# Kernel optimization log

Measured on AMD Instinct MI355X. Metric: run time of the kernel, lower is better.

## Reference

```python
import jax, jax.numpy as jnp
import numpy as np

DIM = 256
KEY_DIM = 16
NUM_HEADS = 8
ATTN_RATIO = 4
RES = (32, 32)
N = RES[0] * RES[1]            # 1024 tokens
D = ATTN_RATIO * KEY_DIM       # 64 per-head value dim
DH = D * NUM_HEADS             # 512
H_QKV = DH + 2 * KEY_DIM * NUM_HEADS  # 768
BATCH = 32
EPS = 1e-5


def _bias_idxs():
    # relative-position offset index table: idx[i,j] = |dr|*W + |dc| (bijective
    # over the res0*res1 unique abs-offset pairs, matching the gather structure)
    r = np.arange(RES[0])
    c = np.arange(RES[1])
    rr, cc = np.meshgrid(r, c, indexing='ij')
    pr = rr.reshape(-1)  # [N]
    pc = cc.reshape(-1)
    dr = np.abs(pr[:, None] - pr[None, :])
    dc = np.abs(pc[:, None] - pc[None, :])
    return jnp.asarray(dr * RES[1] + dc, dtype=jnp.int32)  # [N, N]


def setup_inputs() -> dict:
    key = jax.random.key(0)
    ks = jax.random.split(key, 8)
    s_in = 1.0 / np.sqrt(DIM)
    s_dh = 1.0 / np.sqrt(DH)
    return {
        'x': jax.random.normal(ks[0], (BATCH, N, DIM), jnp.float32),
        'norm_w': jnp.ones((DIM,), jnp.float32),
        'norm_b': jnp.zeros((DIM,), jnp.float32),
        'qkv_w': jax.random.normal(ks[1], (H_QKV, DIM), jnp.float32) * s_in,
        'qkv_b': jnp.zeros((H_QKV,), jnp.float32),
        'proj_w': jax.random.normal(ks[2], (DIM, DH), jnp.float32) * s_dh,
        'proj_b': jnp.zeros((DIM,), jnp.float32),
        'attn_biases': jax.random.normal(ks[3], (NUM_HEADS, RES[0] * RES[1]), jnp.float32) * 0.02,
        'bias_idxs': _bias_idxs(),
    }


def reference(x, norm_w, norm_b, qkv_w, qkv_b, proj_w, proj_b, attn_biases, bias_idxs):
    b, n, _ = x.shape
    scale = KEY_DIM ** -0.5
    # LayerNorm
    mu = jnp.mean(x, axis=-1, keepdims=True)
    var = jnp.mean(jnp.square(x - mu), axis=-1, keepdims=True)
    xn = (x - mu) * jax.lax.rsqrt(var + EPS) * norm_w + norm_b
    # fused qkv projection
    qkv = xn @ qkv_w.T + qkv_b                       # [b, n, H_QKV]
    qkv = qkv.reshape(b, n, NUM_HEADS, 2 * KEY_DIM + D)
    q = qkv[..., :KEY_DIM]                           # [b, n, h, k]
    k = qkv[..., KEY_DIM:2 * KEY_DIM]
    v = qkv[..., 2 * KEY_DIM:]                       # [b, n, h, d]
    # scores + gathered relative-position bias
    bias = attn_biases[:, bias_idxs]                 # [h, n, n]
    attn = jnp.einsum('bnhk,bmhk->bhnm', q, k) * scale + bias
    attn = jax.nn.softmax(attn, axis=-1)
    out = jnp.einsum('bhnm,bmhd->bnhd', attn, v).reshape(b, n, DH)
    return out @ proj_w.T + proj_b                   # [b, n, DIM]
```

## Files before the change

### kernel.cpp

```cpp
#include <hip/hip_runtime.h>
#include <hip/hip_bf16.h>

typedef __bf16 bf16x8 __attribute__((ext_vector_type(8)));
typedef float f32x16 __attribute__((ext_vector_type(16)));
typedef float f32x8 __attribute__((ext_vector_type(8)));
typedef float f32x2 __attribute__((ext_vector_type(2)));
typedef unsigned int u32;

#define MFMA32(a, b, c) __builtin_amdgcn_mfma_f32_32x32x16_bf16((a), (b), (c), 0, 0, 0)

__device__ __forceinline__ f32x16 zero16() {
  f32x16 z;
#pragma unroll
  for (int i = 0; i < 16; ++i) z[i] = 0.f;
  return z;
}

__device__ __forceinline__ unsigned short bfb(float f) {
  __hip_bfloat16 h = __float2bfloat16(f);
  return __builtin_bit_cast(unsigned short, h);
}
__device__ __forceinline__ u32 pk2(float lo, float hi) {
  return (u32)bfb(lo) | ((u32)bfb(hi) << 16);
}
__device__ __forceinline__ u32 pk2h(float lo, float hi) {
  _Float16 a = (_Float16)lo, b = (_Float16)hi;
  return (u32)__builtin_bit_cast(unsigned short, a) |
         ((u32)__builtin_bit_cast(unsigned short, b) << 16);
}
__device__ __forceinline__ bf16x8 ld8(const unsigned short* p) {
  return *reinterpret_cast<const bf16x8*>(p);
}
__device__ __forceinline__ void gld_lds16(const void* g, void* l) {
  __builtin_amdgcn_global_load_lds((const __attribute__((address_space(1))) void*)g,
                                   (__attribute__((address_space(3))) void*)l, 16, 0, 0);
}

__global__ __launch_bounds__(256, 4) void ln_kernel(const float* __restrict__ x,
                                                    const float* __restrict__ nw,
                                                    const float* __restrict__ nb,
                                                    unsigned short* __restrict__ xn) {
  int w = threadIdx.x >> 6, lane = threadIdx.x & 63;
  size_t row = (size_t)blockIdx.x * 4 + w;
  float4 v = reinterpret_cast<const float4*>(x + row * 256)[lane];
  float s = (v.x + v.y) + (v.z + v.w);
  float q = (v.x * v.x + v.y * v.y) + (v.z * v.z + v.w * v.w);
#pragma unroll
  for (int m = 1; m < 64; m <<= 1) {
    s += __shfl_xor(s, m, 64);
    q += __shfl_xor(q, m, 64);
  }
  float mu = s * (1.f / 256.f);
  float var = fmaxf(q * (1.f / 256.f) - mu * mu, 0.f);
  float rs = rsqrtf(var + 1e-5f);
  float4 wv = reinterpret_cast<const float4*>(nw)[lane];
  float4 bv = reinterpret_cast<const float4*>(nb)[lane];
  float o0 = (v.x - mu) * rs * wv.x + bv.x;
  float o1 = (v.y - mu) * rs * wv.y + bv.y;
  float o2 = (v.z - mu) * rs * wv.z + bv.z;
  float o3 = (v.w - mu) * rs * wv.w + bv.w;
  uint2 o = make_uint2(pk2(o0, o1), pk2(o2, o3));
  reinterpret_cast<uint2*>(xn + row * 256)[lane] = o;
}

__global__ __launch_bounds__(256, 4) void wconv_kernel(const float* __restrict__ qkv_w,
                                                       const float* __restrict__ proj_w,
                                                       unsigned short* __restrict__ wq,
                                                       unsigned short* __restrict__ wp) {
  int t = blockIdx.x * 256 + threadIdx.x;
  const int NQ = 49152;
  float4 v;
  unsigned short* dst;
  int idx;
  if (t < NQ) {
    v = reinterpret_cast<const float4*>(qkv_w)[t];
    dst = wq;
    idx = t;
  } else {
    v = reinterpret_cast<const float4*>(proj_w)[t - NQ];
    dst = wp;
    idx = t - NQ;
  }
  uint2 o = make_uint2(pk2(v.x, v.y), pk2(v.z, v.w));
  reinterpret_cast<uint2*>(dst)[idx] = o;
}

__global__ __launch_bounds__(256, 4) void bias_gather(const float* __restrict__ attn_biases,
                                                      const int* __restrict__ bias_idxs,
                                                      unsigned short* __restrict__ biasc) {
  int tt = blockIdx.x * 256 + threadIdx.x;
  int j8 = tt & 3;
  int lane = (tt >> 2) & 63;
  int t = (tt >> 8) & 15;
  int g = (tt >> 12) & 31;
  int h = tt >> 17;
  int q = g * 32 + (lane & 31);
  int lh = lane >> 5;
  int sub = j8 >> 1;
  int rb = (j8 & 1) * 16;
  const int* ir = bias_idxs + q * 1024 + (2 * t + sub) * 32 + 4 * lh + rb;
  int4 i0 = *reinterpret_cast<const int4*>(ir);
  int4 i1 = *reinterpret_cast<const int4*>(ir + 8);
  const float* tb = attn_biases + h * 1024;
  const float L2E = 1.4426950408889634f;
  uint4 o;
  o.x = pk2h(tb[i0.x] * L2E, tb[i0.y] * L2E);
  o.y = pk2h(tb[i0.z] * L2E, tb[i0.w] * L2E);
  o.z = pk2h(tb[i1.x] * L2E, tb[i1.y] * L2E);
  o.w = pk2h(tb[i1.z] * L2E, tb[i1.w] * L2E);
  reinterpret_cast<uint4*>(biasc)[tt] = o;
}

template <int STAGES, int ROWB>
__device__ __forceinline__ void gemm_core(const char* Ag, const char* Bg, char* As, char* Bs,
                                          int m0, int n0, int w, int lane, f32x16 acc[2][2]) {
  int lr = lane & 31, lh = lane >> 5;
  for (int kb = 0; kb < STAGES; ++kb) {
    if (kb) __syncthreads();
#pragma unroll
    for (int i = 0; i < 8; ++i) {
      int ldsoff = (i * 4 + w) * 1024;
      int lflat = ldsoff + lane * 16;
      int row = lflat >> 8;
      int c = (lflat >> 4) & 15;
      int sc_ = (c ^ (row & 7)) << 4;
      gld_lds16(Ag + (size_t)(m0 + row) * ROWB + kb * 256 + sc_, As + ldsoff);
      gld_lds16(Bg + (size_t)(n0 + row) * ROWB + kb * 256 + sc_, Bs + ldsoff);
    }
    asm volatile("s_waitcnt vmcnt(0)" ::: "memory");
    __syncthreads();
    int ra = (w >> 1) * 64 + lr;
    int rb = (w & 1) * 64 + lr;
#pragma unroll
    for (int k16 = 0; k16 < 8; ++k16) {
      bf16x8 af[2], bfr[2];
#pragma unroll
      for (int i = 0; i < 2; ++i) {
        int rowa = ra + i * 32;
        int ca = (((k16 << 1) | lh) ^ (rowa & 7)) << 4;
        af[i] = *reinterpret_cast<const bf16x8*>(As + (rowa << 8) + ca);
        int rowb = rb + i * 32;
        int cb = (((k16 << 1) | lh) ^ (rowb & 7)) << 4;
        bfr[i] = *reinterpret_cast<const bf16x8*>(Bs + (rowb << 8) + cb);
      }
#pragma unroll
      for (int i = 0; i < 2; ++i)
#pragma unroll
        for (int j = 0; j < 2; ++j) acc[i][j] = MFMA32(af[i], bfr[j], acc[i][j]);
    }
  }
}

__global__ __launch_bounds__(256, 2) void qkv_gemm(const unsigned short* __restrict__ xn,
                                                   const unsigned short* __restrict__ wq,
                                                   const float* __restrict__ qkv_b,
                                                   unsigned short* __restrict__ Qb,
                                                   unsigned short* __restrict__ Kb,
                                                   unsigned short* __restrict__ Vt) {
  extern __shared__ char smem[];
  char* As = smem;
  char* Bs = smem + 32768;
  int bid = blockIdx.x;
  int f2 = (bid & 7) * 192 + (bid >> 3);
  int nt = f2 % 6, mt = f2 / 6;
  int tid = threadIdx.x, w = tid >> 6, lane = tid & 63;
  int m0 = mt * 128, n0 = nt * 128;
  f32x16 acc[2][2];
  acc[0][0] = zero16(); acc[0][1] = zero16(); acc[1][0] = zero16(); acc[1][1] = zero16();
  gemm_core<2, 512>((const char*)xn, (const char*)wq, As, Bs, m0, n0, w, lane, acc);
  int lr = lane & 31, lh = lane >> 5;
#pragma unroll
  for (int j = 0; j < 2; ++j) {
    int col = n0 + (w & 1) * 64 + j * 32 + lr;
    int h = col / 96;
    int rr = col - h * 96;
    float bv = qkv_b[col];
#pragma unroll
    for (int i = 0; i < 2; ++i) {
      int rbase = m0 + (w >> 1) * 64 + i * 32 + 4 * lh;
      if (rr < 32) {
        unsigned short* dst0 = (rr < 16) ? Qb : Kb;
        int cc = rr & 15;
#pragma unroll
        for (int r = 0; r < 16; ++r) {
          int n = rbase + (r & 3) + 8 * (r >> 2);
          int b = n >> 10, nn = n & 1023;
          dst0[(((size_t)(b * 8 + h) * 1024 + nn) << 4) + cc] = bfb(acc[i][j][r] + bv);
        }
      } else {
        int d = rr - 32;
#pragma unroll
        for (int g = 0; g < 4; ++g) {
          int n = rbase + 8 * g;
          int b = n >> 10, nn = n & 1023;
          int t = nn >> 5, s0 = nn & 31;
          int s = (s0 & ~12) | ((s0 & 4) << 1) | ((s0 & 8) >> 1);
          size_t addr = ((size_t)(b * 8 + h) << 16) + t * 2048 + (s >> 3) * 512 + d * 8 + (s & 7);
          ushort4 pkv;
          pkv.x = bfb(acc[i][j][4 * g + 0] + bv);
          pkv.y = bfb(acc[i][j][4 * g + 1] + bv);
          pkv.z = bfb(acc[i][j][4 * g + 2] + bv);
          pkv.w = bfb(acc[i][j][4 * g + 3] + bv);
          *reinterpret_cast<ushort4*>(Vt + addr) = pkv;
        }
      }
    }
  }
}

__device__ __forceinline__ void stage_tile(const char* kgB, const char* vgB, char* buf,
                                           int t, int w, int lane) {
  const char* vsrc = vgB + (size_t)t * 8192;
  if (w < 2) {
    gld_lds16(kgB + (size_t)t * 2048 + w * 1024 + lane * 16, buf + w * 1024);
    gld_lds16(vsrc + w * 1024 + lane * 16, buf + 2048 + w * 1024);
    gld_lds16(vsrc + (4 + w) * 1024 + lane * 16, buf + 2048 + (4 + w) * 1024);
  } else {
    gld_lds16(vsrc + w * 1024 + lane * 16, buf + 2048 + w * 1024);
    gld_lds16(vsrc + (4 + w) * 1024 + lane * 16, buf + 2048 + (4 + w) * 1024);
  }
}

__device__ __forceinline__ bf16x8 cvt8(const float* p) {
  f32x8 v;
#pragma unroll
  for (int i = 0; i < 8; ++i) v[i] = p[i];
  return __builtin_convertvector(v, bf16x8);
}

__global__ __launch_bounds__(256, 3) void attn_kernel(const unsigned short* __restrict__ Qb,
                                                      const unsigned short* __restrict__ Kb,
                                                      const unsigned short* __restrict__ Vt,
                                                      const unsigned short* __restrict__ biasc,
                                                      unsigned short* __restrict__ aout) {
  extern __shared__ char smem[];
  int bid = blockIdx.x;
  int f2 = (bid & 7) * 256 + (bid >> 3);
  int qt = f2 & 7, b = (f2 >> 3) & 31, h = f2 >> 8;
  int w = threadIdx.x >> 6, lane = threadIdx.x & 63;
  int lr = lane & 31, lh = lane >> 5;
  int bh = b * 8 + h;
  int qg = qt * 128 + w * 32 + lr;
  bf16x8 qf = ld8(Qb + (((size_t)bh * 1024 + qg) << 4) + lh * 8);
  const char* kgB = (const char*)Kb + ((size_t)bh << 15);
  const char* vgB = (const char*)Vt + ((size_t)bh << 17);
  const char* bgB = (const char*)biasc + ((size_t)((h * 32 + qt * 4 + w) * 1024 + lane) << 6);
  f32x16 acc0 = zero16(), acc1 = zero16();
  f32x2 ls2 = {0.f, 0.f};
  const float SC = 0.25f * 1.4426950408889634f;

  stage_tile(kgB, vgB, smem, 0, w, lane);
  __builtin_amdgcn_sched_barrier(0);
  uint4 cb0 = *reinterpret_cast<const uint4*>(bgB);
  uint4 cb1 = *reinterpret_cast<const uint4*>(bgB + 16);
  uint4 cb2 = *reinterpret_cast<const uint4*>(bgB + 32);
  uint4 cb3 = *reinterpret_cast<const uint4*>(bgB + 48);

#pragma unroll 2
  for (int t = 0; t < 16; ++t) {
    char* cur = smem + (t & 1) * 10240;
    char* nxt = smem + ((t + 1) & 1) * 10240;
    asm volatile("s_waitcnt vmcnt(4)" ::: "memory");
    __builtin_amdgcn_sched_barrier(0);
    __builtin_amdgcn_s_barrier();
    __builtin_amdgcn_sched_barrier(0);
    bf16x8 kf0 = *reinterpret_cast<const bf16x8*>(cur + lr * 32 + lh * 16);
    bf16x8 kf1 = *reinterpret_cast<const bf16x8*>(cur + 1024 + lr * 32 + lh * 16);
    const char* Vs = cur + 2048;
    bf16x8 va00 = *reinterpret_cast<const bf16x8*>(Vs + lh * 1024 + lr * 16);
    bf16x8 va10 = *reinterpret_cast<const bf16x8*>(Vs + (2 + lh) * 1024 + lr * 16);
    bf16x8 va01 = *reinterpret_cast<const bf16x8*>(Vs + lh * 1024 + 512 + lr * 16);
    bf16x8 va11 = *reinterpret_cast<const bf16x8*>(Vs + (2 + lh) * 1024 + 512 + lr * 16);
    bf16x8 vb00 = *reinterpret_cast<const bf16x8*>(Vs + 4096 + lh * 1024 + lr * 16);
    bf16x8 vb10 = *reinterpret_cast<const bf16x8*>(Vs + 4096 + (2 + lh) * 1024 + lr * 16);
    bf16x8 vb01 = *reinterpret_cast<const bf16x8*>(Vs + 4096 + lh * 1024 + 512 + lr * 16);
    bf16x8 vb11 = *reinterpret_cast<const bf16x8*>(Vs + 4096 + (2 + lh) * 1024 + 512 + lr * 16);
    stage_tile(kgB, vgB, nxt, t + 1, w, lane);
    __builtin_amdgcn_sched_barrier(0);
    const char* bp = bgB + (size_t)(t + 1) * 4096;
    uint4 nb0 = *reinterpret_cast<const uint4*>(bp);
    uint4 nb1 = *reinterpret_cast<const uint4*>(bp + 16);
    uint4 nb2 = *reinterpret_cast<const uint4*>(bp + 32);
    uint4 nb3 = *reinterpret_cast<const uint4*>(bp + 48);
    __builtin_amdgcn_s_setprio(1);
    f32x16 st0 = MFMA32(kf0, qf, zero16());
    f32x16 st1 = MFMA32(kf1, qf, zero16());
    union { uint4 u[4]; _Float16 hh[32]; } bb;
    bb.u[0] = cb0; bb.u[1] = cb1; bb.u[2] = cb2; bb.u[3] = cb3;
    float p0[16], p1[16];
#pragma unroll
    for (int r = 0; r < 16; ++r)
      p0[r] = __builtin_amdgcn_exp2f(fmaf(st0[r], SC, (float)bb.hh[r]));
#pragma unroll
    for (int r = 0; r < 16; ++r)
      p1[r] = __builtin_amdgcn_exp2f(fmaf(st1[r], SC, (float)bb.hh[16 + r]));
    bf16x8 a0A = cvt8(p0), a1A = cvt8(p0 + 8);
    bf16x8 a0B = cvt8(p1), a1B = cvt8(p1 + 8);
    acc0 = MFMA32(a0A, va00, acc0);
    acc0 = MFMA32(a1A, va10, acc0);
    acc1 = MFMA32(a0A, va01, acc1);
    acc1 = MFMA32(a1A, va11, acc1);
    acc0 = MFMA32(a0B, vb00, acc0);
    acc0 = MFMA32(a1B, vb10, acc0);
    acc1 = MFMA32(a0B, vb01, acc1);
    acc1 = MFMA32(a1B, vb11, acc1);
    __builtin_amdgcn_s_setprio(0);
#pragma unroll
    for (int i = 0; i < 8; ++i) {
      f32x2 e0 = {p0[2 * i], p0[2 * i + 1]};
      f32x2 e1 = {p1[2 * i], p1[2 * i + 1]};
      ls2 += e0 + e1;
    }
    cb0 = nb0; cb1 = nb1; cb2 = nb2; cb3 = nb3;
  }

  float lsum = ls2[0] + ls2[1];
  float ls = lsum + __shfl_xor(lsum, 32, 64);
  float inv = 1.f / ls;
  size_t obase = (((size_t)b << 10) + qt * 128 + w * 32) * 512 + h * 64;
#pragma unroll
  for (int r = 0; r < 16; ++r) {
    int qrow = (r & 3) + 8 * (r >> 2) + 4 * lh;
    float sc2 = __shfl(inv, qrow, 64);
    aout[obase + (size_t)qrow * 512 + lr] = bfb(acc0[r] * sc2);
    aout[obase + (size_t)qrow * 512 + 32 + lr] = bfb(acc1[r] * sc2);
  }
}

__global__ __launch_bounds__(256, 2) void proj_gemm(const unsigned short* __restrict__ Ain,
                                                    const unsigned short* __restrict__ wp,
                                                    const float* __restrict__ proj_b,
                                                    float* __restrict__ out) {
  extern __shared__ char smem[];
  char* As = smem;
  char* Bs = smem + 32768;
  int bid = blockIdx.x;
  int f2 = (bid & 7) * 64 + (bid >> 3);
  int nt = f2 & 1, mt = f2 >> 1;
  int tid = threadIdx.x, w = tid >> 6, lane = tid & 63;
  int m0 = mt * 128, n0 = nt * 128;
  f32x16 acc[2][2];
  acc[0][0] = zero16(); acc[0][1] = zero16(); acc[1][0] = zero16(); acc[1][1] = zero16();
  gemm_core<4, 1024>((const char*)Ain, (const char*)wp, As, Bs, m0, n0, w, lane, acc);
  int lr = lane & 31, lh = lane >> 5;
#pragma unroll
  for (int j = 0; j < 2; ++j) {
    int col = n0 + (w & 1) * 64 + j * 32 + lr;
    float pbv = proj_b[col];
#pragma unroll
    for (int i = 0; i < 2; ++i) {
      int rbase = m0 + (w >> 1) * 64 + i * 32 + 4 * lh;
#pragma unroll
      for (int r = 0; r < 16; ++r) {
        int n = rbase + (r & 3) + 8 * (r >> 2);
        out[(size_t)n * 256 + col] = acc[i][j][r] + pbv;
      }
    }
  }
}

extern "C" void kernel_launch(void* const* d_in, const int* in_sizes, int n_in,
                              void* d_out, int out_size, void* d_ws, size_t ws_size,
                              hipStream_t stream) {
  const float* x = (const float*)d_in[0];
  const float* norm_w = (const float*)d_in[1];
  const float* norm_b = (const float*)d_in[2];
  const float* qkv_w = (const float*)d_in[3];
  const float* qkv_b = (const float*)d_in[4];
  const float* proj_w = (const float*)d_in[5];
  const float* proj_b = (const float*)d_in[6];
  const float* attn_biases = (const float*)d_in[7];
  const int* bias_idxs = (const int*)d_in[8];
  float* out = (float*)d_out;
  char* ws = (char*)d_ws;
  unsigned short* xn = (unsigned short*)(ws + 0);
  unsigned short* wq = (unsigned short*)(ws + 16777216);
  unsigned short* wp = (unsigned short*)(ws + 17170432);
  unsigned short* Qb = (unsigned short*)(ws + 17432576);
  unsigned short* Kb = (unsigned short*)(ws + 25821184);
  unsigned short* Vt = (unsigned short*)(ws + 34209792);
  unsigned short* biasc = (unsigned short*)(ws + 67764224);
  unsigned short* aout = (unsigned short*)(ws + 84541440);

  ln_kernel<<<8192, 256, 0, stream>>>(x, norm_w, norm_b, xn);
  wconv_kernel<<<320, 256, 0, stream>>>(qkv_w, proj_w, wq, wp);
  bias_gather<<<4096, 256, 0, stream>>>(attn_biases, bias_idxs, biasc);
  qkv_gemm<<<1536, 256, 65536, stream>>>(xn, wq, qkv_b, Qb, Kb, Vt);
  attn_kernel<<<2048, 256, 20480, stream>>>(Qb, Kb, Vt, biasc, aout);
  proj_gemm<<<512, 256, 65536, stream>>>(aout, wp, proj_b, out);
}
```

Baseline: 137.5 us.

## Fold softmax scale into Q and preload fp32 bias as MFMA accumulator

The softmax scale (times log2 e) is folded into Q in the QKV GEMM epilogue. The relative-position bias is now stored as fp32 in the exact MFMA accumulator layout, so the QK^T MFMA starts from the bias instead of zero. This drops the per-element fma and fp16-to-fp32 conversion in the attention inner loop. In exchange the bias buffer is twice as large, each iteration issues twice as many bias loads, and the wait count is raised to 8. The workspace is also rearranged so xn and aout share memory.

```diff
diff --git a/kernel.cpp b/kernel.cpp
--- a/kernel.cpp
+++ b/kernel.cpp
@@ -22,11 +22,6 @@
 }
 __device__ __forceinline__ u32 pk2(float lo, float hi) {
   return (u32)bfb(lo) | ((u32)bfb(hi) << 16);
-}
-__device__ __forceinline__ u32 pk2h(float lo, float hi) {
-  _Float16 a = (_Float16)lo, b = (_Float16)hi;
-  return (u32)__builtin_bit_cast(unsigned short, a) |
-         ((u32)__builtin_bit_cast(unsigned short, b) << 16);
 }
 __device__ __forceinline__ bf16x8 ld8(const unsigned short* p) {
   return *reinterpret_cast<const bf16x8*>(p);
@@ -87,28 +82,26 @@
 
 __global__ __launch_bounds__(256, 4) void bias_gather(const float* __restrict__ attn_biases,
                                                       const int* __restrict__ bias_idxs,
-                                                      unsigned short* __restrict__ biasc) {
+                                                      float* __restrict__ biasf) {
   int tt = blockIdx.x * 256 + threadIdx.x;
-  int j8 = tt & 3;
-  int lane = (tt >> 2) & 63;
+  int rh = tt & 1;
+  int lane = (tt >> 1) & 63;
+  int sub = (tt >> 7) & 1;
   int t = (tt >> 8) & 15;
   int g = (tt >> 12) & 31;
   int h = tt >> 17;
   int q = g * 32 + (lane & 31);
   int lh = lane >> 5;
-  int sub = j8 >> 1;
-  int rb = (j8 & 1) * 16;
-  const int* ir = bias_idxs + q * 1024 + (2 * t + sub) * 32 + 4 * lh + rb;
+  const int* ir = bias_idxs + q * 1024 + (2 * t + sub) * 32 + 4 * lh + 16 * rh;
   int4 i0 = *reinterpret_cast<const int4*>(ir);
   int4 i1 = *reinterpret_cast<const int4*>(ir + 8);
   const float* tb = attn_biases + h * 1024;
   const float L2E = 1.4426950408889634f;
-  uint4 o;
-  o.x = pk2h(tb[i0.x] * L2E, tb[i0.y] * L2E);
-  o.y = pk2h(tb[i0.z] * L2E, tb[i0.w] * L2E);
-  o.z = pk2h(tb[i1.x] * L2E, tb[i1.y] * L2E);
-  o.w = pk2h(tb[i1.z] * L2E, tb[i1.w] * L2E);
-  reinterpret_cast<uint4*>(biasc)[tt] = o;
+  float4 o0 = make_float4(tb[i0.x] * L2E, tb[i0.y] * L2E, tb[i0.z] * L2E, tb[i0.w] * L2E);
+  float4 o1 = make_float4(tb[i1.x] * L2E, tb[i1.y] * L2E, tb[i1.z] * L2E, tb[i1.w] * L2E);
+  float4* dst = reinterpret_cast<float4*>(biasf) + ((size_t)(tt >> 1) * 4 + rh * 2);
+  dst[0] = o0;
+  dst[1] = o1;
 }
 
 template <int STAGES, int ROWB>
@@ -180,12 +173,13 @@
       int rbase = m0 + (w >> 1) * 64 + i * 32 + 4 * lh;
       if (rr < 32) {
         unsigned short* dst0 = (rr < 16) ? Qb : Kb;
+        float scl = (rr < 16) ? 0.3606737602222409f : 1.0f;
         int cc = rr & 15;
 #pragma unroll
         for (int r = 0; r < 16; ++r) {
           int n = rbase + (r & 3) + 8 * (r >> 2);
           int b = n >> 10, nn = n & 1023;
-          dst0[(((size_t)(b * 8 + h) * 1024 + nn) << 4) + cc] = bfb(acc[i][j][r] + bv);
+          dst0[(((size_t)(b * 8 + h) * 1024 + nn) << 4) + cc] = bfb((acc[i][j][r] + bv) * scl);
         }
       } else {
         int d = rr - 32;
@@ -231,7 +225,7 @@
 __global__ __launch_bounds__(256, 3) void attn_kernel(const unsigned short* __restrict__ Qb,
                                                       const unsigned short* __restrict__ Kb,
                                                       const unsigned short* __restrict__ Vt,
-                                                      const unsigned short* __restrict__ biasc,
+                                                      const float* __restrict__ biasf,
                                                       unsigned short* __restrict__ aout) {
   extern __shared__ char smem[];
   int bid = blockIdx.x;
@@ -244,10 +238,9 @@
   bf16x8 qf = ld8(Qb + (((size_t)bh * 1024 + qg) << 4) + lh * 8);
   const char* kgB = (const char*)Kb + ((size_t)bh << 15);
   const char* vgB = (const char*)Vt + ((size_t)bh << 17);
-  const char* bgB = (const char*)biasc + ((size_t)((h * 32 + qt * 4 + w) * 1024 + lane) << 6);
+  const char* bgB = (const char*)biasf + ((size_t)(h * 32 + qt * 4 + w) << 17) + lane * 64;
   f32x16 acc0 = zero16(), acc1 = zero16();
   f32x2 ls2 = {0.f, 0.f};
-  const float SC = 0.25f * 1.4426950408889634f;
 
   stage_tile(kgB, vgB, smem, 0, w, lane);
   __builtin_amdgcn_sched_barrier(0);
@@ -255,12 +248,16 @@
   uint4 cb1 = *reinterpret_cast<const uint4*>(bgB + 16);
   uint4 cb2 = *reinterpret_cast<const uint4*>(bgB + 32);
   uint4 cb3 = *reinterpret_cast<const uint4*>(bgB + 48);
+  uint4 cb4 = *reinterpret_cast<const uint4*>(bgB + 4096);
+  uint4 cb5 = *reinterpret_cast<const uint4*>(bgB + 4096 + 16);
+  uint4 cb6 = *reinterpret_cast<const uint4*>(bgB + 4096 + 32);
+  uint4 cb7 = *reinterpret_cast<const uint4*>(bgB + 4096 + 48);
 
 #pragma unroll 2
   for (int t = 0; t < 16; ++t) {
     char* cur = smem + (t & 1) * 10240;
     char* nxt = smem + ((t + 1) & 1) * 10240;
-    asm volatile("s_waitcnt vmcnt(4)" ::: "memory");
+    asm volatile("s_waitcnt vmcnt(8)" ::: "memory");
     __builtin_amdgcn_sched_barrier(0);
     __builtin_amdgcn_s_barrier();
     __builtin_amdgcn_sched_barrier(0);
@@ -277,23 +274,26 @@
     bf16x8 vb11 = *reinterpret_cast<const bf16x8*>(Vs + 4096 + (2 + lh) * 1024 + 512 + lr * 16);
     stage_tile(kgB, vgB, nxt, t + 1, w, lane);
     __builtin_amdgcn_sched_barrier(0);
-    const char* bp = bgB + (size_t)(t + 1) * 4096;
+    const char* bp = bgB + (size_t)(t + 1) * 8192;
     uint4 nb0 = *reinterpret_cast<const uint4*>(bp);
     uint4 nb1 = *reinterpret_cast<const uint4*>(bp + 16);
     uint4 nb2 = *reinterpret_cast<const uint4*>(bp + 32);
     uint4 nb3 = *reinterpret_cast<const uint4*>(bp + 48);
+    uint4 nb4 = *reinterpret_cast<const uint4*>(bp + 4096);
+    uint4 nb5 = *reinterpret_cast<const uint4*>(bp + 4096 + 16);
+    uint4 nb6 = *reinterpret_cast<const uint4*>(bp + 4096 + 32);
+    uint4 nb7 = *reinterpret_cast<const uint4*>(bp + 4096 + 48);
     __builtin_amdgcn_s_setprio(1);
-    f32x16 st0 = MFMA32(kf0, qf, zero16());
-    f32x16 st1 = MFMA32(kf1, qf, zero16());
-    union { uint4 u[4]; _Float16 hh[32]; } bb;
-    bb.u[0] = cb0; bb.u[1] = cb1; bb.u[2] = cb2; bb.u[3] = cb3;
+    union BU { uint4 u[4]; f32x16 v; };
+    BU c0u; c0u.u[0] = cb0; c0u.u[1] = cb1; c0u.u[2] = cb2; c0u.u[3] = cb3;
+    BU c1u; c1u.u[0] = cb4; c1u.u[1] = cb5; c1u.u[2] = cb6; c1u.u[3] = cb7;
+    f32x16 st0 = MFMA32(kf0, qf, c0u.v);
+    f32x16 st1 = MFMA32(kf1, qf, c1u.v);
     float p0[16], p1[16];
 #pragma unroll
-    for (int r = 0; r < 16; ++r)
-      p0[r] = __builtin_amdgcn_exp2f(fmaf(st0[r], SC, (float)bb.hh[r]));
-#pragma unroll
-    for (int r = 0; r < 16; ++r)
-      p1[r] = __builtin_amdgcn_exp2f(fmaf(st1[r], SC, (float)bb.hh[16 + r]));
+    for (int r = 0; r < 16; ++r) p0[r] = __builtin_amdgcn_exp2f(st0[r]);
+#pragma unroll
+    for (int r = 0; r < 16; ++r) p1[r] = __builtin_amdgcn_exp2f(st1[r]);
     bf16x8 a0A = cvt8(p0), a1A = cvt8(p0 + 8);
     bf16x8 a0B = cvt8(p1), a1B = cvt8(p1 + 8);
     acc0 = MFMA32(a0A, va00, acc0);
@@ -312,6 +312,7 @@
       ls2 += e0 + e1;
     }
     cb0 = nb0; cb1 = nb1; cb2 = nb2; cb3 = nb3;
+    cb4 = nb4; cb5 = nb5; cb6 = nb6; cb7 = nb7;
   }
 
   float lsum = ls2[0] + ls2[1];
@@ -373,19 +374,19 @@
   const int* bias_idxs = (const int*)d_in[8];
   float* out = (float*)d_out;
   char* ws = (char*)d_ws;
-  unsigned short* xn = (unsigned short*)(ws + 0);
-  unsigned short* wq = (unsigned short*)(ws + 16777216);
-  unsigned short* wp = (unsigned short*)(ws + 17170432);
-  unsigned short* Qb = (unsigned short*)(ws + 17432576);
-  unsigned short* Kb = (unsigned short*)(ws + 25821184);
-  unsigned short* Vt = (unsigned short*)(ws + 34209792);
-  unsigned short* biasc = (unsigned short*)(ws + 67764224);
+  unsigned short* Qb = (unsigned short*)(ws + 0);
+  unsigned short* Kb = (unsigned short*)(ws + 8388608);
+  unsigned short* Vt = (unsigned short*)(ws + 16777216);
+  float* biasf = (float*)(ws + 50331648);
+  unsigned short* wp = (unsigned short*)(ws + 83886080);
+  unsigned short* wq = (unsigned short*)(ws + 84148224);
+  unsigned short* xn = (unsigned short*)(ws + 84541440);
   unsigned short* aout = (unsigned short*)(ws + 84541440);
 
   ln_kernel<<<8192, 256, 0, stream>>>(x, norm_w, norm_b, xn);
   wconv_kernel<<<320, 256, 0, stream>>>(qkv_w, proj_w, wq, wp);
-  bias_gather<<<4096, 256, 0, stream>>>(attn_biases, bias_idxs, biasc);
+  bias_gather<<<4096, 256, 0, stream>>>(attn_biases, bias_idxs, biasf);
   qkv_gemm<<<1536, 256, 65536, stream>>>(xn, wq, qkv_b, Qb, Kb, Vt);
-  attn_kernel<<<2048, 256, 20480, stream>>>(Qb, Kb, Vt, biasc, aout);
+  attn_kernel<<<2048, 256, 20480, stream>>>(Qb, Kb, Vt, biasf, aout);
   proj_gemm<<<512, 256, 65536, stream>>>(aout, wp, proj_b, out);
 }
```

Result: slower. 158.1 us (+15.0%).

## Process two 32-row query tiles per wave to reuse staged K/V tiles

Applied to the files above, without the earlier changes.

Each attention wave now handles 64 query rows (two 32-row MFMA tiles) instead of 32, so each block covers 256 queries and the grid halves. Every K/V tile staged in LDS is reused across twice as many queries, which halves global K/V traffic and the barrier count per query. Bias loads are no longer prefetched one iteration ahead; they are issued after the barrier, and the wait now drains all outstanding loads (vmcnt(0)). Register pressure rises, so occupancy drops from 3 to 2 blocks per SIMD target, and fewer blocks are in flight.

```diff
diff --git a/kernel.cpp b/kernel.cpp
--- a/kernel.cpp
+++ b/kernel.cpp
@@ -228,42 +228,50 @@
   return __builtin_convertvector(v, bf16x8);
 }
 
-__global__ __launch_bounds__(256, 3) void attn_kernel(const unsigned short* __restrict__ Qb,
+__global__ __launch_bounds__(256, 2) void attn_kernel(const unsigned short* __restrict__ Qb,
                                                       const unsigned short* __restrict__ Kb,
                                                       const unsigned short* __restrict__ Vt,
                                                       const unsigned short* __restrict__ biasc,
                                                       unsigned short* __restrict__ aout) {
   extern __shared__ char smem[];
   int bid = blockIdx.x;
-  int f2 = (bid & 7) * 256 + (bid >> 3);
-  int qt = f2 & 7, b = (f2 >> 3) & 31, h = f2 >> 8;
+  int f2 = (bid & 7) * 128 + (bid >> 3);
+  int qt = f2 & 3, b = (f2 >> 2) & 31, h = f2 >> 7;
   int w = threadIdx.x >> 6, lane = threadIdx.x & 63;
   int lr = lane & 31, lh = lane >> 5;
   int bh = b * 8 + h;
-  int qg = qt * 128 + w * 32 + lr;
-  bf16x8 qf = ld8(Qb + (((size_t)bh * 1024 + qg) << 4) + lh * 8);
+  int q0 = qt * 256 + w * 64 + lr;
+  bf16x8 qf0 = ld8(Qb + (((size_t)bh * 1024 + q0) << 4) + lh * 8);
+  bf16x8 qf1 = ld8(Qb + (((size_t)bh * 1024 + q0 + 32) << 4) + lh * 8);
   const char* kgB = (const char*)Kb + ((size_t)bh << 15);
   const char* vgB = (const char*)Vt + ((size_t)bh << 17);
-  const char* bgB = (const char*)biasc + ((size_t)((h * 32 + qt * 4 + w) * 1024 + lane) << 6);
-  f32x16 acc0 = zero16(), acc1 = zero16();
-  f32x2 ls2 = {0.f, 0.f};
+  int g0 = qt * 8 + w * 2;
+  const char* bgB0 = (const char*)biasc + ((size_t)((h * 32 + g0) * 1024 + lane) << 6);
+  const char* bgB1 = bgB0 + ((size_t)1024 << 6);
+  f32x16 acc00 = zero16(), acc01 = zero16();
+  f32x16 acc10 = zero16(), acc11 = zero16();
+  f32x2 ls0 = {0.f, 0.f}, ls1 = {0.f, 0.f};
   const float SC = 0.25f * 1.4426950408889634f;
 
   stage_tile(kgB, vgB, smem, 0, w, lane);
-  __builtin_amdgcn_sched_barrier(0);
-  uint4 cb0 = *reinterpret_cast<const uint4*>(bgB);
-  uint4 cb1 = *reinterpret_cast<const uint4*>(bgB + 16);
-  uint4 cb2 = *reinterpret_cast<const uint4*>(bgB + 32);
-  uint4 cb3 = *reinterpret_cast<const uint4*>(bgB + 48);
-
-#pragma unroll 2
+
   for (int t = 0; t < 16; ++t) {
     char* cur = smem + (t & 1) * 10240;
     char* nxt = smem + ((t + 1) & 1) * 10240;
-    asm volatile("s_waitcnt vmcnt(4)" ::: "memory");
+    asm volatile("s_waitcnt vmcnt(0)" ::: "memory");
     __builtin_amdgcn_sched_barrier(0);
     __builtin_amdgcn_s_barrier();
     __builtin_amdgcn_sched_barrier(0);
+    const char* bp0 = bgB0 + (size_t)t * 4096;
+    const char* bp1 = bgB1 + (size_t)t * 4096;
+    uint4 b00 = *reinterpret_cast<const uint4*>(bp0);
+    uint4 b01 = *reinterpret_cast<const uint4*>(bp0 + 16);
+    uint4 b02 = *reinterpret_cast<const uint4*>(bp0 + 32);
+    uint4 b03 = *reinterpret_cast<const uint4*>(bp0 + 48);
+    uint4 b10 = *reinterpret_cast<const uint4*>(bp1);
+    uint4 b11 = *reinterpret_cast<const uint4*>(bp1 + 16);
+    uint4 b12 = *reinterpret_cast<const uint4*>(bp1 + 32);
+    uint4 b13 = *reinterpret_cast<const uint4*>(bp1 + 48);
     bf16x8 kf0 = *reinterpret_cast<const bf16x8*>(cur + lr * 32 + lh * 16);
     bf16x8 kf1 = *reinterpret_cast<const bf16x8*>(cur + 1024 + lr * 32 + lh * 16);
     const char* Vs = cur + 2048;
@@ -277,53 +285,88 @@
     bf16x8 vb11 = *reinterpret_cast<const bf16x8*>(Vs + 4096 + (2 + lh) * 1024 + 512 + lr * 16);
     stage_tile(kgB, vgB, nxt, t + 1, w, lane);
     __builtin_amdgcn_sched_barrier(0);
-    const char* bp = bgB + (size_t)(t + 1) * 4096;
-    uint4 nb0 = *reinterpret_cast<const uint4*>(bp);
-    uint4 nb1 = *reinterpret_cast<const uint4*>(bp + 16);
-    uint4 nb2 = *reinterpret_cast<const uint4*>(bp + 32);
-    uint4 nb3 = *reinterpret_cast<const uint4*>(bp + 48);
     __builtin_amdgcn_s_setprio(1);
-    f32x16 st0 = MFMA32(kf0, qf, zero16());
-    f32x16 st1 = MFMA32(kf1, qf, zero16());
-    union { uint4 u[4]; _Float16 hh[32]; } bb;
-    bb.u[0] = cb0; bb.u[1] = cb1; bb.u[2] = cb2; bb.u[3] = cb3;
-    float p0[16], p1[16];
-#pragma unroll
-    for (int r = 0; r < 16; ++r)
-      p0[r] = __builtin_amdgcn_exp2f(fmaf(st0[r], SC, (float)bb.hh[r]));
-#pragma unroll
-    for (int r = 0; r < 16; ++r)
-      p1[r] = __builtin_amdgcn_exp2f(fmaf(st1[r], SC, (float)bb.hh[16 + r]));
-    bf16x8 a0A = cvt8(p0), a1A = cvt8(p0 + 8);
-    bf16x8 a0B = cvt8(p1), a1B = cvt8(p1 + 8);
-    acc0 = MFMA32(a0A, va00, acc0);
-    acc0 = MFMA32(a1A, va10, acc0);
-    acc1 = MFMA32(a0A, va01, acc1);
-    acc1 = MFMA32(a1A, va11, acc1);
-    acc0 = MFMA32(a0B, vb00, acc0);
-    acc0 = MFMA32(a1B, vb10, acc0);
-    acc1 = MFMA32(a0B, vb01, acc1);
-    acc1 = MFMA32(a1B, vb11, acc1);
+    f32x16 stA0 = MFMA32(kf0, qf0, zero16());
+    f32x16 stB0 = MFMA32(kf1, qf0, zero16());
+    f32x16 stA1 = MFMA32(kf0, qf1, zero16());
+    f32x16 stB1 = MFMA32(kf1, qf1, zero16());
+    union BB { uint4 u[2]; _Float16 hh[16]; };
+    {
+      BB bb; bb.u[0] = b00; bb.u[1] = b01;
+      float p[16];
+#pragma unroll
+      for (int r = 0; r < 16; ++r)
+        p[r] = __builtin_amdgcn_exp2f(fmaf(stA0[r], SC, (float)bb.hh[r]));
+      bf16x8 a0 = cvt8(p), a1 = cvt8(p + 8);
+      acc00 = MFMA32(a0, va00, acc00);
+      acc01 = MFMA32(a0, va01, acc01);
+      acc00 = MFMA32(a1, va10, acc00);
+      acc01 = MFMA32(a1, va11, acc01);
+#pragma unroll
+      for (int i = 0; i < 8; ++i) { f32x2 e = {p[2 * i], p[2 * i + 1]}; ls0 += e; }
+    }
+    {
+      BB bb; bb.u[0] = b02; bb.u[1] = b03;
+      float p[16];
+#pragma unroll
+      for (int r = 0; r < 16; ++r)
+        p[r] = __builtin_amdgcn_exp2f(fmaf(stB0[r], SC, (float)bb.hh[r]));
+      bf16x8 a0 = cvt8(p), a1 = cvt8(p + 8);
+      acc00 = MFMA32(a0, vb00, acc00);
+      acc01 = MFMA32(a0, vb01, acc01);
+      acc00 = MFMA32(a1, vb10, acc00);
+      acc01 = MFMA32(a1, vb11, acc01);
+#pragma unroll
+      for (int i = 0; i < 8; ++i) { f32x2 e = {p[2 * i], p[2 * i + 1]}; ls0 += e; }
+    }
+    {
+      BB bb; bb.u[0] = b10; bb.u[1] = b11;
+      float p[16];
+#pragma unroll
+      for (int r = 0; r < 16; ++r)
+        p[r] = __builtin_amdgcn_exp2f(fmaf(stA1[r], SC, (float)bb.hh[r]));
+      bf16x8 a0 = cvt8(p), a1 = cvt8(p + 8);
+      acc10 = MFMA32(a0, va00, acc10);
+      acc11 = MFMA32(a0, va01, acc11);
+      acc10 = MFMA32(a1, va10, acc10);
+      acc11 = MFMA32(a1, va11, acc11);
+#pragma unroll
+      for (int i = 0; i < 8; ++i) { f32x2 e = {p[2 * i], p[2 * i + 1]}; ls1 += e; }
+    }
+    {
+      BB bb; bb.u[0] = b12; bb.u[1] = b13;
+      float p[16];
+#pragma unroll
+      for (int r = 0; r < 16; ++r)
+        p[r] = __builtin_amdgcn_exp2f(fmaf(stB1[r], SC, (float)bb.hh[r]));
+      bf16x8 a0 = cvt8(p), a1 = cvt8(p + 8);
+      acc10 = MFMA32(a0, vb00, acc10);
+      acc11 = MFMA32(a0, vb01, acc11);
+      acc10 = MFMA32(a1, vb10, acc10);
+      acc11 = MFMA32(a1, vb11, acc11);
+#pragma unroll
+      for (int i = 0; i < 8; ++i) { f32x2 e = {p[2 * i], p[2 * i + 1]}; ls1 += e; }
+    }
     __builtin_amdgcn_s_setprio(0);
-#pragma unroll
-    for (int i = 0; i < 8; ++i) {
-      f32x2 e0 = {p0[2 * i], p0[2 * i + 1]};
-      f32x2 e1 = {p1[2 * i], p1[2 * i + 1]};
-      ls2 += e0 + e1;
-    }
-    cb0 = nb0; cb1 = nb1; cb2 = nb2; cb3 = nb3;
-  }
-
-  float lsum = ls2[0] + ls2[1];
-  float ls = lsum + __shfl_xor(lsum, 32, 64);
-  float inv = 1.f / ls;
-  size_t obase = (((size_t)b << 10) + qt * 128 + w * 32) * 512 + h * 64;
+  }
+
+  float l0 = ls0[0] + ls0[1];
+  float s0 = l0 + __shfl_xor(l0, 32, 64);
+  float inv0 = 1.f / s0;
+  float l1 = ls1[0] + ls1[1];
+  float s1 = l1 + __shfl_xor(l1, 32, 64);
+  float inv1 = 1.f / s1;
+  size_t ob0 = (((size_t)b << 10) + qt * 256 + w * 64) * 512 + h * 64;
+  size_t ob1 = ob0 + (size_t)32 * 512;
 #pragma unroll
   for (int r = 0; r < 16; ++r) {
     int qrow = (r & 3) + 8 * (r >> 2) + 4 * lh;
-    float sc2 = __shfl(inv, qrow, 64);
-    aout[obase + (size_t)qrow * 512 + lr] = bfb(acc0[r] * sc2);
-    aout[obase + (size_t)qrow * 512 + 32 + lr] = bfb(acc1[r] * sc2);
+    float c0 = __shfl(inv0, qrow, 64);
+    aout[ob0 + (size_t)qrow * 512 + lr] = bfb(acc00[r] * c0);
+    aout[ob0 + (size_t)qrow * 512 + 32 + lr] = bfb(acc01[r] * c0);
+    float c1 = __shfl(inv1, qrow, 64);
+    aout[ob1 + (size_t)qrow * 512 + lr] = bfb(acc10[r] * c1);
+    aout[ob1 + (size_t)qrow * 512 + 32 + lr] = bfb(acc11[r] * c1);
   }
 }
 
@@ -386,6 +429,6 @@
   wconv_kernel<<<320, 256, 0, stream>>>(qkv_w, proj_w, wq, wp);
   bias_gather<<<4096, 256, 0, stream>>>(attn_biases, bias_idxs, biasc);
   qkv_gemm<<<1536, 256, 65536, stream>>>(xn, wq, qkv_b, Qb, Kb, Vt);
-  attn_kernel<<<2048, 256, 20480, stream>>>(Qb, Kb, Vt, biasc, aout);
+  attn_kernel<<<1024, 256, 20480, stream>>>(Qb, Kb, Vt, biasc, aout);
   proj_gemm<<<512, 256, 65536, stream>>>(aout, wp, proj_b, out);
 }
```

New measurement: 130.0 us. 5.5% less time.
